# Performance work log

Hardware: AMD Instinct MI355X
Metric: run time of the kernel (lower is better)

## Reference

```python
import jax, jax.numpy as jnp
import numpy as np

N_HEAD = 4
D_K = 512 // N_HEAD  # 128
PAD = 5  # (kernel 11 - 1) // 2, sanm_shift=0 -> symmetric 'same' padding
EPS = 1e-5


def layer_norm(x, w, b):
    m = jnp.mean(x, axis=-1, keepdims=True)
    v = jnp.mean(jnp.square(x - m), axis=-1, keepdims=True)
    return (x - m) * jax.lax.rsqrt(v + EPS) * w + b


def setup_inputs() -> dict:
    key = jax.random.key(0)
    ks = jax.random.split(key, 8)
    B, T, D = 64, 218, 512
    s = 0.05
    return {
        "x": jax.random.normal(ks[0], (B, T, D), jnp.float32),
        "masks": jnp.ones((B, T), jnp.float32),
        "ln0_w": jax.random.uniform(ks[1], (D,), jnp.float32, 0.9, 1.1),
        "ln0_b": jnp.zeros((D,), jnp.float32),
        "ln1_w": jax.random.uniform(ks[2], (D,), jnp.float32, 0.9, 1.1),
        "ln1_b": jnp.zeros((D,), jnp.float32),
        "qkv_w": jax.random.normal(ks[3], (D, 3 * D), jnp.float32) * s,
        "qkv_b": jnp.zeros((3 * D,), jnp.float32),
        "out_w": jax.random.normal(ks[4], (D, D), jnp.float32) * s,
        "out_b": jnp.zeros((D,), jnp.float32),
        "fsmn_w": jax.random.normal(ks[5], (D, D, 11), jnp.float32) * s,
        "w1": jax.random.normal(ks[6], (D, 4 * D), jnp.float32) * s,
        "b1": jnp.zeros((4 * D,), jnp.float32),
        "w2": jax.random.normal(ks[7], (4 * D, D), jnp.float32) * s,
        "b2": jnp.zeros((D,), jnp.float32),
    }


def encoder_layer(x, masks, ln0_w, ln0_b, ln1_w, ln1_b, qkv_w, qkv_b,
                  out_w, out_b, fsmn_w, w1, b1, w2, b2):
    B, T, D = x.shape
    m = masks[..., None]  # (B,T,1)

    # ---- self_attn_sanm block ----
    residual = x
    h = layer_norm(x, ln0_w, ln0_b)
    qkv = h @ qkv_w + qkv_b                      # (B,T,3D)
    q, k, v = jnp.split(qkv, 3, axis=-1)         # each (B,T,D)

    # FSMN memory branch on (masked) v: Conv1d(512,512,11), 'same' padding
    vm = v * m
    # torch conv weight (out,in,k) -> jax 'WIO' kernel (k,in,out)
    kern = jnp.transpose(fsmn_w, (2, 1, 0))
    fsmn = jax.lax.conv_general_dilated(
        vm, kern, window_strides=(1,), padding=[(PAD, PAD)],
        dimension_numbers=("NWC", "WIO", "NWC"))
    fsmn = (fsmn + vm) * m                       # (B,T,D)

    # multi-head attention
    def heads(t):  # (B,T,D) -> (B,H,T,dk)
        return t.reshape(B, T, N_HEAD, D_K).transpose(0, 2, 1, 3)
    qh, kh, vh = heads(q), heads(k), heads(v)
    scores = jnp.einsum("bhqd,bhkd->bhqk", qh, kh) / np.sqrt(D_K)
    neg = jnp.finfo(scores.dtype).min
    scores = jnp.where(masks[:, None, None, :] > 0, scores, neg)
    attn = jax.nn.softmax(scores, axis=-1)
    ctx = jnp.einsum("bhqk,bhkd->bhqd", attn, vh)
    ctx = ctx.transpose(0, 2, 1, 3).reshape(B, T, D)
    att_out = ctx @ out_w + out_b + fsmn
    x = residual + att_out

    # ---- feed-forward block (512 -> 2048 -> 512, relu) ----
    residual = x
    h = layer_norm(x, ln1_w, ln1_b)
    ffn = jax.nn.relu(h @ w1 + b1) @ w2 + b2
    return residual + ffn


def reference(x, masks, ln0_w, ln0_b, ln1_w, ln1_b, qkv_w, qkv_b,
              out_w, out_b, fsmn_w, w1, b1, w2, b2):
    return encoder_layer(x, masks, ln0_w, ln0_b, ln1_w, ln1_b,
                         qkv_w, qkv_b, out_w, out_b, fsmn_w, w1, b1, w2, b2)
```

## Files before the change

### kernel.cpp

```cpp
#include <hip/hip_runtime.h>
#include <cstdint>

#define B_   64
#define T_   218
#define TP_  228
#define D_   512
#define M_   13952
#define MT_  109
#define H_   4
#define DK_  128
#define PW_  224
#define N3_  1536
#define DFF_ 2048
#define KC_  5632
#define KH_  2816

typedef unsigned short u16;
using short8 = __attribute__((ext_vector_type(8))) short;
using f32x4  = __attribute__((ext_vector_type(4))) float;

__device__ __forceinline__ float b2f(u16 u) {
  union { float f; uint32_t i; } v; v.i = ((uint32_t)u) << 16; return v.f;
}
__device__ __forceinline__ u16 f2b(float f) {
  union { float f; uint32_t i; } v; v.f = f;
  uint32_t r = v.i + 0x7fffu + ((v.i >> 16) & 1u);
  return (u16)(r >> 16);
}
union U8 { uint4 v; u16 u[8]; };

__device__ __forceinline__ void gll16(const u16* g, u16* l) {
  __builtin_amdgcn_global_load_lds(
      (const __attribute__((address_space(1))) unsigned int*)g,
      (__attribute__((address_space(3))) unsigned int*)l, 16, 0, 0);
}

template<int MODE>
__global__ __launch_bounds__(256, 2)
void gemm_u(const u16* __restrict__ A, int sA, const u16* __restrict__ Bt, int sB,
            const float* __restrict__ bias, const float* __restrict__ conv0,
            const u16* __restrict__ vmp, u16* __restrict__ vmout,
            const float* __restrict__ add_f, void* __restrict__ outp,
            int N, int K, int ntc, const float* __restrict__ masks)
{
  __shared__ u16 As[128 * 32];
  __shared__ u16 Bs[128 * 32];

  int mt, nt, zb = 0;
  if (MODE == 5) {
    mt = blockIdx.x; nt = 0; zb = blockIdx.z;
  } else if (MODE == 4) {
    const int j = blockIdx.x & 7;
    nt = j & 3; zb = j >> 2;
    mt = blockIdx.x >> 3;
  } else {
    const int xcd = blockIdx.x & 7;
    const int lin = blockIdx.x >> 3;
    nt = lin % ntc;
    mt = xcd + 8 * (lin / ntc);
    if (mt >= MT_) return;
  }
  const int m0 = mt * 128, n0 = nt * 128;

  const int tid = threadIdx.x, lane = tid & 63, w = tid >> 6;
  const int wm = (w >> 1) * 64, wn = (w & 1) * 64;
  const int l15 = lane & 15, qd = lane >> 4;

  const u16* Ab  = A;
  const u16* Btb = Bt;
  if (MODE == 5) { Ab = A + (size_t)zb * 256 * PW_; Btb = Bt + (size_t)zb * 128 * PW_; }

  const int rl = lane >> 2, ce = (lane & 3) * 8;
  const int r0 = m0 + w * 16 + rl, r1 = r0 + 64;
  size_t aoff0, aoff1, bkoff = 0;
  if (MODE == 4) {
    const int b0r = r0 / T_, t0r = r0 - b0r * T_;
    const int b1r = r1 / T_, t1r = r1 - b1r * T_;
    aoff0 = ((size_t)b0r * TP_ + t0r) * D_ + (size_t)zb * KH_;
    aoff1 = ((size_t)b1r * TP_ + t1r) * D_ + (size_t)zb * KH_;
    bkoff = (size_t)zb * KH_;
  } else {
    aoff0 = (size_t)r0 * sA;
    aoff1 = (size_t)r1 * sA;
  }
  const u16* ag0 = Ab + aoff0 + ce;
  const u16* ag1 = Ab + aoff1 + ce;
  const u16* bg0 = Btb + (size_t)(n0 + w * 16 + rl) * sB + bkoff + ce;
  const u16* bg1 = bg0 + (size_t)64 * sB;
  u16* lA0 = As + w * 512;
  u16* lA1 = As + 2048 + w * 512;
  u16* lB0 = Bs + w * 512;
  u16* lB1 = Bs + 2048 + w * 512;

  const f32x4 z4 = {0.f, 0.f, 0.f, 0.f};
  f32x4 acc[4][4];
#pragma unroll
  for (int i = 0; i < 4; i++)
#pragma unroll
    for (int j = 0; j < 4; j++) acc[i][j] = z4;

  for (int k0 = 0; k0 < K; k0 += 32) {
    __syncthreads();
    gll16(ag0 + k0, lA0);
    gll16(ag1 + k0, lA1);
    gll16(bg0 + k0, lB0);
    gll16(bg1 + k0, lB1);
    __syncthreads();
    short8 af[4], bf[4];
#pragma unroll
    for (int mi = 0; mi < 4; mi++) af[mi] = *(const short8*)&As[(wm + mi * 16 + l15) * 32 + qd * 8];
#pragma unroll
    for (int ni = 0; ni < 4; ni++) bf[ni] = *(const short8*)&Bs[(wn + ni * 16 + l15) * 32 + qd * 8];
#pragma unroll
    for (int mi = 0; mi < 4; mi++)
#pragma unroll
      for (int ni = 0; ni < 4; ni++)
        acc[mi][ni] = __builtin_amdgcn_mfma_f32_16x16x32_bf16(af[mi], bf[ni], acc[mi][ni], 0, 0, 0);
  }

#pragma unroll
  for (int ni = 0; ni < 4; ni++) {
    const int c = n0 + wn + ni * 16 + l15;
    const float bv = (MODE == 4 || MODE == 5) ? 0.f : bias[c];
#pragma unroll
    for (int mi = 0; mi < 4; mi++) {
#pragma unroll
      for (int rg = 0; rg < 4; rg++) {
        const int r = m0 + wm + mi * 16 + qd * 4 + rg;
        float v = acc[mi][ni][rg] + bv;
        if (MODE == 0) {
          ((u16*)outp)[(size_t)r * N + c] = f2b(v);
          if (c >= 1024) {
            const int b = r / T_, t = r - b * T_;
            vmout[((size_t)b * TP_ + t + 5) * D_ + (c - 1024)] = f2b(v * masks[r]);
          }
        } else if (MODE == 1) {
          const size_t idx = (size_t)r * N + c;
          const int b = r / T_, t = r - b * T_;
          const float m  = masks[r];
          const float cv = conv0[idx] + conv0[idx + (size_t)M_ * 512];
          const float vm = b2f(vmp[((size_t)b * TP_ + t + 5) * D_ + c]);
          ((float*)outp)[idx] = v + (cv + vm) * m + add_f[idx];
        } else if (MODE == 2) {
          ((u16*)outp)[(size_t)r * N + c] = f2b(fmaxf(v, 0.f));
        } else if (MODE == 3) {
          const size_t idx = (size_t)r * N + c;
          ((float*)outp)[idx] = v + add_f[idx];
        } else if (MODE == 4) {
          ((float*)outp)[(size_t)zb * ((size_t)M_ * 512) + (size_t)r * N + c] = v;
        } else {
          const int t = r;
          if (t < T_) {
            const int b = zb >> 2, h = zb & 3;
            ((u16*)outp)[((size_t)b * T_ + t) * D_ + h * DK_ + c] = f2b(v);
          }
        }
      }
    }
  }
}

__global__ __launch_bounds__(256, 2)
void attn_scores(const u16* __restrict__ qkv, const float* __restrict__ masks,
                 u16* __restrict__ P)
{
  __shared__ u16 Qs[64][136];
  __shared__ u16 Ks[64][136];
  __shared__ float red0[4][64];
  __shared__ float red1[4][64];
  const int tid = threadIdx.x, lane = tid & 63, w = tid >> 6;
  const int l15 = lane & 15, qd = lane >> 4;
  const int bh = blockIdx.y, b = bh >> 2, h = bh & 3;
  const int q0 = blockIdx.x * 64;
  const uint4 uz = make_uint4(0, 0, 0, 0);

#pragma unroll
  for (int i = 0; i < 4; i++) {
    const int ch = tid + i * 256;
    const int row = ch >> 4, cg = (ch & 15) * 8;
    const int t = q0 + row;
    uint4 v = uz;
    if (t < T_) v = *(const uint4*)(qkv + ((size_t)b * T_ + t) * N3_ + h * DK_ + cg);
    *(uint4*)&Qs[row][cg] = v;
  }

  const f32x4 z4 = {0.f, 0.f, 0.f, 0.f};
  f32x4 acc[4][4];
#pragma unroll
  for (int i = 0; i < 4; i++)
#pragma unroll
    for (int j = 0; j < 4; j++) acc[i][j] = z4;

#pragma unroll
  for (int kc = 0; kc < 4; kc++) {
    __syncthreads();
#pragma unroll
    for (int i = 0; i < 4; i++) {
      const int ch = tid + i * 256;
      const int row = ch >> 4, cg = (ch & 15) * 8;
      const int t = kc * 64 + row;
      uint4 v = uz;
      if (t < T_) v = *(const uint4*)(qkv + ((size_t)b * T_ + t) * N3_ + D_ + h * DK_ + cg);
      *(uint4*)&Ks[row][cg] = v;
    }
    __syncthreads();
#pragma unroll
    for (int ks = 0; ks < 4; ks++) {
      short8 bf = *(const short8*)&Ks[w * 16 + l15][ks * 32 + qd * 8];
#pragma unroll
      for (int mi = 0; mi < 4; mi++) {
        short8 af = *(const short8*)&Qs[mi * 16 + l15][ks * 32 + qd * 8];
        acc[kc][mi] = __builtin_amdgcn_mfma_f32_16x16x32_bf16(af, bf, acc[kc][mi], 0, 0, 0);
      }
    }
  }

  const float scale = 0.08838834764831845f;
  const int colb = w * 16 + l15;
  bool valid[4];
#pragma unroll
  for (int kc = 0; kc < 4; kc++) {
    const int col = kc * 64 + colb;
    valid[kc] = (col < T_) && (masks[b * T_ + col] > 0.f);
  }

  float mx[4][4], sm[4][4];
#pragma unroll
  for (int mi = 0; mi < 4; mi++)
#pragma unroll
    for (int rg = 0; rg < 4; rg++) {
      float m = -1e30f;
#pragma unroll
      for (int kc = 0; kc < 4; kc++)
        if (valid[kc]) m = fmaxf(m, acc[kc][mi][rg] * scale);
      for (int d = 1; d < 16; d <<= 1) m = fmaxf(m, __shfl_xor(m, d, 64));
      mx[mi][rg] = m;
    }
  if (l15 == 0) {
#pragma unroll
    for (int mi = 0; mi < 4; mi++)
#pragma unroll
      for (int rg = 0; rg < 4; rg++) red0[w][mi * 16 + qd * 4 + rg] = mx[mi][rg];
  }
  __syncthreads();
#pragma unroll
  for (int mi = 0; mi < 4; mi++)
#pragma unroll
    for (int rg = 0; rg < 4; rg++) {
      const int r = mi * 16 + qd * 4 + rg;
      mx[mi][rg] = fmaxf(fmaxf(red0[0][r], red0[1][r]), fmaxf(red0[2][r], red0[3][r]));
    }
#pragma unroll
  for (int mi = 0; mi < 4; mi++)
#pragma unroll
    for (int rg = 0; rg < 4; rg++) {
      float s = 0.f;
#pragma unroll
      for (int kc = 0; kc < 4; kc++)
        if (valid[kc]) s += __expf(acc[kc][mi][rg] * scale - mx[mi][rg]);
      for (int d = 1; d < 16; d <<= 1) s += __shfl_xor(s, d, 64);
      sm[mi][rg] = s;
    }
  if (l15 == 0) {
#pragma unroll
    for (int mi = 0; mi < 4; mi++)
#pragma unroll
      for (int rg = 0; rg < 4; rg++) red1[w][mi * 16 + qd * 4 + rg] = sm[mi][rg];
  }
  __syncthreads();
#pragma unroll
  for (int mi = 0; mi < 4; mi++)
#pragma unroll
    for (int rg = 0; rg < 4; rg++) {
      const int r = mi * 16 + qd * 4 + rg;
      const int gq = q0 + r;
      const float inv = 1.f / (red1[0][r] + red1[1][r] + red1[2][r] + red1[3][r]);
#pragma unroll
      for (int kc = 0; kc < 4; kc++) {
        const int col = kc * 64 + colb;
        if (col < PW_) {
          const float p = valid[kc] ? __expf(acc[kc][mi][rg] * scale - mx[mi][rg]) * inv : 0.f;
          P[((size_t)bh * 256 + gq) * PW_ + col] = f2b(p);
        }
      }
    }
}

__global__ __launch_bounds__(256)
void ln_k(const float* __restrict__ x, const float* __restrict__ wgt,
          const float* __restrict__ bia, u16* __restrict__ outp)
{
  const int lane = threadIdx.x & 63, wv = threadIdx.x >> 6;
  const size_t row = (size_t)blockIdx.x * 4 + wv;
  const float* rp = x + row * D_ + lane * 8;
  float v[8], s = 0.f, s2 = 0.f;
  float4 r0 = *(const float4*)rp;
  float4 r1 = *(const float4*)(rp + 4);
  v[0] = r0.x; v[1] = r0.y; v[2] = r0.z; v[3] = r0.w;
  v[4] = r1.x; v[5] = r1.y; v[6] = r1.z; v[7] = r1.w;
#pragma unroll
  for (int i = 0; i < 8; i++) { s += v[i]; s2 += v[i] * v[i]; }
  for (int d = 1; d < 64; d <<= 1) { s += __shfl_xor(s, d, 64); s2 += __shfl_xor(s2, d, 64); }
  const float mean = s * (1.f / 512.f);
  const float var  = s2 * (1.f / 512.f) - mean * mean;
  const float rs   = rsqrtf(var + 1e-5f);
  float4 w0 = *(const float4*)(wgt + lane * 8);
  float4 w1 = *(const float4*)(wgt + lane * 8 + 4);
  float4 b0 = *(const float4*)(bia + lane * 8);
  float4 b1 = *(const float4*)(bia + lane * 8 + 4);
  const float wv8[8] = {w0.x, w0.y, w0.z, w0.w, w1.x, w1.y, w1.z, w1.w};
  const float bv8[8] = {b0.x, b0.y, b0.z, b0.w, b1.x, b1.y, b1.z, b1.w};
  U8 o;
#pragma unroll
  for (int i = 0; i < 8; i++)
    o.u[i] = f2b((v[i] - mean) * rs * wv8[i] + bv8[i]);
  *(uint4*)(outp + row * D_ + lane * 8) = o.v;
}

__global__ __launch_bounds__(256)
void prep_all(const float* __restrict__ qkv_w, const float* __restrict__ out_w,
              const float* __restrict__ w1, const float* __restrict__ w2,
              const float* __restrict__ fsmn_w,
              u16* __restrict__ qkv_wT, u16* __restrict__ out_wT,
              u16* __restrict__ w1T, u16* __restrict__ w2T,
              u16* __restrict__ fsmnW2, u16* __restrict__ vmpad)
{
  const int bid = blockIdx.x;
  if (bid < 3072) {
    const float* src; u16* dst; int K, N, tb;
    if (bid < 768)       { src = qkv_w; dst = qkv_wT; K = 512;  N = 1536; tb = bid; }
    else if (bid < 1024) { src = out_w; dst = out_wT; K = 512;  N = 512;  tb = bid - 768; }
    else if (bid < 2048) { src = w1;    dst = w1T;    K = 512;  N = 2048; tb = bid - 1024; }
    else                 { src = w2;    dst = w2T;    K = 2048; N = 512;  tb = bid - 2048; }
    const int ktiles = K / 32;
    const int k0 = (tb % ktiles) * 32, n0 = (tb / ktiles) * 32;
    __shared__ float tile[32][33];
    const int x = threadIdx.x & 31, y = threadIdx.x >> 5;
#pragma unroll
    for (int j = 0; j < 4; j++)
      tile[y + j * 8][x] = src[(size_t)(k0 + y + j * 8) * N + n0 + x];
    __syncthreads();
#pragma unroll
    for (int j = 0; j < 4; j++)
      dst[(size_t)(n0 + y + j * 8) * K + k0 + x] = f2b(tile[x][y + j * 8]);
  } else if (bid < 4096) {
    const int idx = (bid - 3072) * 256 + threadIdx.x;
    const int o = idx >> 9, i = idx & 511;
    const float* s = fsmn_w + (size_t)idx * 11;
#pragma unroll
    for (int tap = 0; tap < 11; ++tap)
      fsmnW2[(size_t)o * KC_ + tap * 512 + i] = f2b(s[tap]);
  } else {
    const int e8 = (bid - 4096) * 256 + threadIdx.x;
    const int e  = e8 * 8;
    const int c  = e & 511;
    const int pr = e >> 9;
    const int b  = pr / 10, j = pr % 10;
    const int row = (j < 5) ? j : (218 + j);
    *(uint4*)(vmpad + ((size_t)b * TP_ + row) * D_ + c) = make_uint4(0, 0, 0, 0);
  }
}

__global__ void fill_vt(const u16* __restrict__ qkv, u16* __restrict__ Vt)
{
  __shared__ u16 tile[32][33];
  const int bh = blockIdx.z, b = bh >> 2, h = bh & 3;
  const int kv0 = blockIdx.x * 32, d0 = blockIdx.y * 32;
  const int x = threadIdx.x & 31, y = threadIdx.x >> 5;
#pragma unroll
  for (int j = 0; j < 4; j++) {
    const int kv = kv0 + y + j * 8;
    u16 v = 0;
    if (kv < T_) v = qkv[((size_t)b * T_ + kv) * N3_ + 1024 + h * DK_ + d0 + x];
    tile[y + j * 8][x] = v;
  }
  __syncthreads();
#pragma unroll
  for (int j = 0; j < 4; j++) {
    const int d = d0 + y + j * 8;
    Vt[((size_t)bh * 128 + d) * PW_ + kv0 + x] = tile[x][y + j * 8];
  }
}

extern "C" void kernel_launch(void* const* d_in, const int* in_sizes, int n_in,
                              void* d_out, int out_size, void* d_ws, size_t ws_size,
                              hipStream_t stream)
{
  const float* x      = (const float*)d_in[0];
  const float* masks  = (const float*)d_in[1];
  const float* ln0_w  = (const float*)d_in[2];
  const float* ln0_b  = (const float*)d_in[3];
  const float* ln1_w  = (const float*)d_in[4];
  const float* ln1_b  = (const float*)d_in[5];
  const float* qkv_w  = (const float*)d_in[6];
  const float* qkv_b  = (const float*)d_in[7];
  const float* out_w  = (const float*)d_in[8];
  const float* out_b  = (const float*)d_in[9];
  const float* fsmn_w = (const float*)d_in[10];
  const float* w1     = (const float*)d_in[11];
  const float* b1     = (const float*)d_in[12];
  const float* w2     = (const float*)d_in[13];
  const float* b2     = (const float*)d_in[14];
  float* outp = (float*)d_out;
  u16* ws   = (u16*)d_ws;

  size_t off = 0;
  u16* qkv_wT = ws + off; off += (size_t)1536 * 512;
  u16* out_wT = ws + off; off += (size_t)512 * 512;
  u16* w1T    = ws + off; off += (size_t)2048 * 512;
  u16* w2T    = ws + off; off += (size_t)512 * 2048;
  u16* fsmnW2 = ws + off; off += (size_t)512 * KC_;
  u16* slotA  = ws + off; off += (size_t)M_ * 512;
  u16* qkvb   = ws + off; off += (size_t)M_ * 1536;
  u16* vmpad  = ws + off; off += (size_t)B_ * TP_ * 512;
  u16* regionX= ws + off;
  u16* Pbuf   = regionX;
  u16* Vtbuf  = regionX + (size_t)256 * 256 * PW_;
  float* convacc = (float*)(Vtbuf + (size_t)256 * 128 * PW_);
  u16* hid    = regionX;
  u16* h1     = qkvb;
  float* x1   = (float*)(qkvb + (size_t)M_ * 512);

  prep_all<<<4256, 256, 0, stream>>>(qkv_w, out_w, w1, w2, fsmn_w,
                                     qkv_wT, out_wT, w1T, w2T, fsmnW2, vmpad);
  ln_k<<<M_ / 4, 256, 0, stream>>>(x, ln0_w, ln0_b, slotA);
  gemm_u<0><<<8 * 14 * 12, 256, 0, stream>>>(
      slotA, 512, qkv_wT, 512, qkv_b, nullptr, nullptr, vmpad, nullptr, qkvb,
      1536, 512, 12, masks);
  gemm_u<4><<<MT_ * 8, 256, 0, stream>>>(
      vmpad, 0, fsmnW2, KC_, nullptr, nullptr, nullptr, nullptr, nullptr, convacc,
      512, KH_, 4, nullptr);
  fill_vt<<<dim3(7, 4, 256), 256, 0, stream>>>(qkvb, Vtbuf);
  attn_scores<<<dim3(4, 256), 256, 0, stream>>>(qkvb, masks, Pbuf);
  gemm_u<5><<<dim3(2, 1, 256), 256, 0, stream>>>(
      Pbuf, PW_, Vtbuf, PW_, nullptr, nullptr, nullptr, nullptr, nullptr, slotA,
      128, PW_, 1, nullptr);
  gemm_u<1><<<8 * 14 * 4, 256, 0, stream>>>(
      slotA, 512, out_wT, 512, out_b, convacc, vmpad, nullptr, x, x1,
      512, 512, 4, masks);
  ln_k<<<M_ / 4, 256, 0, stream>>>(x1, ln1_w, ln1_b, h1);
  gemm_u<2><<<8 * 14 * 16, 256, 0, stream>>>(
      h1, 512, w1T, 512, b1, nullptr, nullptr, nullptr, nullptr, hid,
      2048, 512, 16, nullptr);
  gemm_u<3><<<8 * 14 * 4, 256, 0, stream>>>(
      hid, 2048, w2T, 2048, b2, nullptr, nullptr, nullptr, x1, outp,
      512, 2048, 4, nullptr);
}
```

Measured before the change: 511.9 us.

## Fuse attention softmax with PV product and store FSMN partials as bf16

Attention scores, softmax and the P·V product now run in one kernel. P stays in shared memory, and V is transposed into LDS inside that kernel, so the P and Vt buffers in global memory, the fill_vt kernel and the mode-5 GEMM all go away. Separately, the FSMN conv split-K partial sums are written as bf16 instead of fp32, which halves that traffic. The cost is extra LDS use, scalar transposing stores of V into LDS, and lower precision on the conv partials.

Result: no change. 504.9 us (-1.4%).

```diff
diff --git a/kernel.cpp b/kernel.cpp
--- a/kernel.cpp
+++ b/kernel.cpp
@@ -38,7 +38,7 @@
 template<int MODE>
 __global__ __launch_bounds__(256, 2)
 void gemm_u(const u16* __restrict__ A, int sA, const u16* __restrict__ Bt, int sB,
-            const float* __restrict__ bias, const float* __restrict__ conv0,
+            const float* __restrict__ bias, const u16* __restrict__ convb,
             const u16* __restrict__ vmp, u16* __restrict__ vmout,
             const float* __restrict__ add_f, void* __restrict__ outp,
             int N, int K, int ntc, const float* __restrict__ masks)
@@ -47,9 +47,7 @@
   __shared__ u16 Bs[128 * 32];
 
   int mt, nt, zb = 0;
-  if (MODE == 5) {
-    mt = blockIdx.x; nt = 0; zb = blockIdx.z;
-  } else if (MODE == 4) {
+  if (MODE == 4) {
     const int j = blockIdx.x & 7;
     nt = j & 3; zb = j >> 2;
     mt = blockIdx.x >> 3;
@@ -65,10 +63,6 @@
   const int tid = threadIdx.x, lane = tid & 63, w = tid >> 6;
   const int wm = (w >> 1) * 64, wn = (w & 1) * 64;
   const int l15 = lane & 15, qd = lane >> 4;
-
-  const u16* Ab  = A;
-  const u16* Btb = Bt;
-  if (MODE == 5) { Ab = A + (size_t)zb * 256 * PW_; Btb = Bt + (size_t)zb * 128 * PW_; }
 
   const int rl = lane >> 2, ce = (lane & 3) * 8;
   const int r0 = m0 + w * 16 + rl, r1 = r0 + 64;
@@ -83,9 +77,9 @@
     aoff0 = (size_t)r0 * sA;
     aoff1 = (size_t)r1 * sA;
   }
-  const u16* ag0 = Ab + aoff0 + ce;
-  const u16* ag1 = Ab + aoff1 + ce;
-  const u16* bg0 = Btb + (size_t)(n0 + w * 16 + rl) * sB + bkoff + ce;
+  const u16* ag0 = A + aoff0 + ce;
+  const u16* ag1 = A + aoff1 + ce;
+  const u16* bg0 = Bt + (size_t)(n0 + w * 16 + rl) * sB + bkoff + ce;
   const u16* bg1 = bg0 + (size_t)64 * sB;
   u16* lA0 = As + w * 512;
   u16* lA1 = As + 2048 + w * 512;
@@ -121,7 +115,7 @@
 #pragma unroll
   for (int ni = 0; ni < 4; ni++) {
     const int c = n0 + wn + ni * 16 + l15;
-    const float bv = (MODE == 4 || MODE == 5) ? 0.f : bias[c];
+    const float bv = (MODE == 4) ? 0.f : bias[c];
 #pragma unroll
     for (int mi = 0; mi < 4; mi++) {
 #pragma unroll
@@ -138,7 +132,7 @@
           const size_t idx = (size_t)r * N + c;
           const int b = r / T_, t = r - b * T_;
           const float m  = masks[r];
-          const float cv = conv0[idx] + conv0[idx + (size_t)M_ * 512];
+          const float cv = b2f(convb[idx]) + b2f(convb[idx + (size_t)M_ * 512]);
           const float vm = b2f(vmp[((size_t)b * TP_ + t + 5) * D_ + c]);
           ((float*)outp)[idx] = v + (cv + vm) * m + add_f[idx];
         } else if (MODE == 2) {
@@ -146,14 +140,8 @@
         } else if (MODE == 3) {
           const size_t idx = (size_t)r * N + c;
           ((float*)outp)[idx] = v + add_f[idx];
-        } else if (MODE == 4) {
-          ((float*)outp)[(size_t)zb * ((size_t)M_ * 512) + (size_t)r * N + c] = v;
         } else {
-          const int t = r;
-          if (t < T_) {
-            const int b = zb >> 2, h = zb & 3;
-            ((u16*)outp)[((size_t)b * T_ + t) * D_ + h * DK_ + c] = f2b(v);
-          }
+          ((u16*)outp)[(size_t)zb * ((size_t)M_ * 512) + (size_t)r * N + c] = f2b(v);
         }
       }
     }
@@ -161,13 +149,17 @@
 }
 
 __global__ __launch_bounds__(256, 2)
-void attn_scores(const u16* __restrict__ qkv, const float* __restrict__ masks,
-                 u16* __restrict__ P)
+void attn_fused(const u16* __restrict__ qkv, const float* __restrict__ masks,
+                u16* __restrict__ ctx)
 {
-  __shared__ u16 Qs[64][136];
-  __shared__ u16 Ks[64][136];
+  __shared__ u16 smem[29696];
   __shared__ float red0[4][64];
   __shared__ float red1[4][64];
+  u16* Qs = smem;
+  u16* Ks = smem + 64 * 136;
+  u16* Ps = smem;
+  u16* Vs = smem + 64 * 232;
+
   const int tid = threadIdx.x, lane = tid & 63, w = tid >> 6;
   const int l15 = lane & 15, qd = lane >> 4;
   const int bh = blockIdx.y, b = bh >> 2, h = bh & 3;
@@ -181,7 +173,7 @@
     const int t = q0 + row;
     uint4 v = uz;
     if (t < T_) v = *(const uint4*)(qkv + ((size_t)b * T_ + t) * N3_ + h * DK_ + cg);
-    *(uint4*)&Qs[row][cg] = v;
+    *(uint4*)&Qs[row * 136 + cg] = v;
   }
 
   const f32x4 z4 = {0.f, 0.f, 0.f, 0.f};
@@ -201,15 +193,15 @@
       const int t = kc * 64 + row;
       uint4 v = uz;
       if (t < T_) v = *(const uint4*)(qkv + ((size_t)b * T_ + t) * N3_ + D_ + h * DK_ + cg);
-      *(uint4*)&Ks[row][cg] = v;
+      *(uint4*)&Ks[row * 136 + cg] = v;
     }
     __syncthreads();
 #pragma unroll
     for (int ks = 0; ks < 4; ks++) {
-      short8 bf = *(const short8*)&Ks[w * 16 + l15][ks * 32 + qd * 8];
+      short8 bf = *(const short8*)&Ks[(w * 16 + l15) * 136 + ks * 32 + qd * 8];
 #pragma unroll
       for (int mi = 0; mi < 4; mi++) {
-        short8 af = *(const short8*)&Qs[mi * 16 + l15][ks * 32 + qd * 8];
+        short8 af = *(const short8*)&Qs[(mi * 16 + l15) * 136 + ks * 32 + qd * 8];
         acc[kc][mi] = __builtin_amdgcn_mfma_f32_16x16x32_bf16(af, bf, acc[kc][mi], 0, 0, 0);
       }
     }
@@ -224,7 +216,7 @@
     valid[kc] = (col < T_) && (masks[b * T_ + col] > 0.f);
   }
 
-  float mx[4][4], sm[4][4];
+  float mx[4][4];
 #pragma unroll
   for (int mi = 0; mi < 4; mi++)
 #pragma unroll
@@ -250,6 +242,7 @@
       const int r = mi * 16 + qd * 4 + rg;
       mx[mi][rg] = fmaxf(fmaxf(red0[0][r], red0[1][r]), fmaxf(red0[2][r], red0[3][r]));
     }
+  float sm[4][4];
 #pragma unroll
   for (int mi = 0; mi < 4; mi++)
 #pragma unroll
@@ -273,17 +266,54 @@
 #pragma unroll
     for (int rg = 0; rg < 4; rg++) {
       const int r = mi * 16 + qd * 4 + rg;
-      const int gq = q0 + r;
       const float inv = 1.f / (red1[0][r] + red1[1][r] + red1[2][r] + red1[3][r]);
 #pragma unroll
       for (int kc = 0; kc < 4; kc++) {
         const int col = kc * 64 + colb;
         if (col < PW_) {
           const float p = valid[kc] ? __expf(acc[kc][mi][rg] * scale - mx[mi][rg]) * inv : 0.f;
-          P[((size_t)bh * 256 + gq) * PW_ + col] = f2b(p);
+          Ps[r * 232 + col] = f2b(p);
         }
       }
     }
+
+  const int kvg = tid >> 4, dg = tid & 15;
+#pragma unroll
+  for (int half = 0; half < 2; ++half) {
+    __syncthreads();
+#pragma unroll
+    for (int r = 0; r < 14; ++r) {
+      const int kv = r * 16 + kvg;
+      ushort4 vv = make_ushort4(0, 0, 0, 0);
+      if (kv < T_)
+        vv = *(const ushort4*)(qkv + ((size_t)b * T_ + kv) * N3_ + 1024 + h * DK_ + half * 64 + dg * 4);
+      Vs[(dg * 4 + 0) * 232 + kv] = vv.x;
+      Vs[(dg * 4 + 1) * 232 + kv] = vv.y;
+      Vs[(dg * 4 + 2) * 232 + kv] = vv.z;
+      Vs[(dg * 4 + 3) * 232 + kv] = vv.w;
+    }
+    __syncthreads();
+    f32x4 a2[4] = {z4, z4, z4, z4};
+#pragma unroll
+    for (int k0 = 0; k0 < 7; ++k0) {
+      short8 af = *(const short8*)&Ps[(w * 16 + l15) * 232 + k0 * 32 + qd * 8];
+#pragma unroll
+      for (int nt = 0; nt < 4; ++nt) {
+        short8 bf = *(const short8*)&Vs[(nt * 16 + l15) * 232 + k0 * 32 + qd * 8];
+        a2[nt] = __builtin_amdgcn_mfma_f32_16x16x32_bf16(af, bf, a2[nt], 0, 0, 0);
+      }
+    }
+    const int tb = q0 + w * 16 + qd * 4;
+#pragma unroll
+    for (int nt = 0; nt < 4; ++nt) {
+      const int d = h * DK_ + half * 64 + nt * 16 + l15;
+#pragma unroll
+      for (int rg = 0; rg < 4; ++rg) {
+        const int tt = tb + rg;
+        if (tt < T_) ctx[((size_t)b * T_ + tt) * D_ + d] = f2b(a2[nt][rg]);
+      }
+    }
+  }
 }
 
 __global__ __launch_bounds__(256)
@@ -358,27 +388,6 @@
     const int b  = pr / 10, j = pr % 10;
     const int row = (j < 5) ? j : (218 + j);
     *(uint4*)(vmpad + ((size_t)b * TP_ + row) * D_ + c) = make_uint4(0, 0, 0, 0);
-  }
-}
-
-__global__ void fill_vt(const u16* __restrict__ qkv, u16* __restrict__ Vt)
-{
-  __shared__ u16 tile[32][33];
-  const int bh = blockIdx.z, b = bh >> 2, h = bh & 3;
-  const int kv0 = blockIdx.x * 32, d0 = blockIdx.y * 32;
-  const int x = threadIdx.x & 31, y = threadIdx.x >> 5;
-#pragma unroll
-  for (int j = 0; j < 4; j++) {
-    const int kv = kv0 + y + j * 8;
-    u16 v = 0;
-    if (kv < T_) v = qkv[((size_t)b * T_ + kv) * N3_ + 1024 + h * DK_ + d0 + x];
-    tile[y + j * 8][x] = v;
-  }
-  __syncthreads();
-#pragma unroll
-  for (int j = 0; j < 4; j++) {
-    const int d = d0 + y + j * 8;
-    Vt[((size_t)bh * 128 + d) * PW_ + kv0 + x] = tile[x][y + j * 8];
   }
 }
 
@@ -414,12 +423,10 @@
   u16* qkvb   = ws + off; off += (size_t)M_ * 1536;
   u16* vmpad  = ws + off; off += (size_t)B_ * TP_ * 512;
   u16* regionX= ws + off;
-  u16* Pbuf   = regionX;
-  u16* Vtbuf  = regionX + (size_t)256 * 256 * PW_;
-  float* convacc = (float*)(Vtbuf + (size_t)256 * 128 * PW_);
-  u16* hid    = regionX;
-  u16* h1     = qkvb;
-  float* x1   = (float*)(qkvb + (size_t)M_ * 512);
+  u16* convacc = regionX;
+  u16* hid     = regionX;
+  u16* h1      = qkvb;
+  float* x1    = (float*)(qkvb + (size_t)M_ * 512);
 
   prep_all<<<4256, 256, 0, stream>>>(qkv_w, out_w, w1, w2, fsmn_w,
                                      qkv_wT, out_wT, w1T, w2T, fsmnW2, vmpad);
@@ -430,11 +437,7 @@
   gemm_u<4><<<MT_ * 8, 256, 0, stream>>>(
       vmpad, 0, fsmnW2, KC_, nullptr, nullptr, nullptr, nullptr, nullptr, convacc,
       512, KH_, 4, nullptr);
-  fill_vt<<<dim3(7, 4, 256), 256, 0, stream>>>(qkvb, Vtbuf);
-  attn_scores<<<dim3(4, 256), 256, 0, stream>>>(qkvb, masks, Pbuf);
-  gemm_u<5><<<dim3(2, 1, 256), 256, 0, stream>>>(
-      Pbuf, PW_, Vtbuf, PW_, nullptr, nullptr, nullptr, nullptr, nullptr, slotA,
-      128, PW_, 1, nullptr);
+  attn_fused<<<dim3(4, 256), 256, 0, stream>>>(qkvb, masks, slotA);
   gemm_u<1><<<8 * 14 * 4, 256, 0, stream>>>(
       slotA, 512, out_wT, 512, out_b, convacc, vmpad, nullptr, x, x1,
       512, 512, 4, masks);
```
